# Performance work log

Measured on AMD Instinct MI355X. Metric: run time of the kernel, lower is better.

Reference implementation:

```python
import jax, jax.numpy as jnp
import numpy as np

L, B, E, H, NE, K = 1024, 8, 512, 8, 8, 2
HD = E // H
SLOPE = 0.01  # LeakyReLU default negative slope
EPS = 1e-5    # LayerNorm eps


def _lin(x, w, b):
    return x @ w.T + b


def _ln(x, g, b):
    m = x.mean(-1, keepdims=True)
    v = ((x - m) ** 2).mean(-1, keepdims=True)
    return (x - m) / jnp.sqrt(v + EPS) * g + b


def _leaky(x):
    return jnp.where(x >= 0, x, SLOPE * x)


def setup_inputs() -> dict:
    key = jax.random.key(0)
    ks = jax.random.split(key, 16)
    def n(k, shape, s=0.02):
        return (jax.random.normal(k, shape) * s).astype(jnp.float32)
    z = lambda *s: jnp.zeros(s, jnp.float32)
    o = lambda *s: jnp.ones(s, jnp.float32)
    return {
        "x": jax.random.normal(ks[0], (L, B, E), jnp.float32),
        "wq": n(ks[1], (E, E)), "bq": z(E),
        "wk": n(ks[2], (E, E)), "bk": z(E),
        "wv": n(ks[3], (E, E)), "bv": z(E),
        "in_w": n(ks[4], (3 * E, E)), "in_b": z(3 * E),
        "out_w": n(ks[5], (E, E)), "out_b": z(E),
        "ln1_g": o(E), "ln1_b": z(E),
        "ln2_g": o(E), "ln2_b": z(E),
        "sh_w": n(ks[6], (E, E)), "sh_b": z(E),
        "gate_w": n(ks[7], (NE, E)), "gate_b": z(NE),
        "exp_w": n(ks[8], (NE, E, E)), "exp_b": z(NE, E),
    }


def reference(x, wq, bq, wk, bk, wv, bv, in_w, in_b, out_w, out_b,
              ln1_g, ln1_b, ln2_g, ln2_b, sh_w, sh_b,
              gate_w, gate_b, exp_w, exp_b):
    # --- outer QKV projections (to_q/to_k/to_v) ---
    q = _lin(x, wq, bq); k = _lin(x, wk, bk); v = _lin(x, wv, bv)
    # --- nn.MultiheadAttention internal in_proj + SDPA + out_proj ---
    wqi, wki, wvi = jnp.split(in_w, 3, axis=0)
    bqi, bki, bvi = jnp.split(in_b, 3)
    q = _lin(q, wqi, bqi); k = _lin(k, wki, bki); v = _lin(v, wvi, bvi)
    heads = lambda t: t.reshape(L, B, H, HD).transpose(1, 2, 0, 3)  # (B,H,L,HD)
    qh, kh, vh = heads(q), heads(k), heads(v)
    att = jax.nn.softmax(
        jnp.einsum('bhqd,bhkd->bhqk', qh, kh) / np.float32(np.sqrt(HD)), axis=-1)
    ao = jnp.einsum('bhqk,bhkd->bhqd', att, vh).transpose(2, 0, 1, 3).reshape(L, B, E)
    ao = _lin(ao, out_w, out_b)
    x1 = _ln(x + ao, ln1_g, ln1_b)
    # --- top-k MoE (vectorized dense expert eval + gather/combine) ---
    probs = jax.nn.softmax(_lin(x1, gate_w, gate_b), axis=-1)     # (L,B,NE)
    topv, topi = jax.lax.top_k(probs, K)                          # (L,B,K)
    wts = topv / topv.sum(-1, keepdims=True)
    allout = _leaky(jnp.einsum('lbe,noe->lbno', x1, exp_w) + exp_b)  # (L,B,NE,E)
    sel = jnp.take_along_axis(allout, jnp.broadcast_to(topi[..., None], (L, B, K, E)), axis=2)
    moe_out = (wts[..., None] * sel).sum(axis=2)                  # (L,B,E)
    # Switch-style load-balance auxiliary loss
    mask = jax.nn.one_hot(topi, NE, dtype=x1.dtype).sum(axis=2)   # (L,B,NE)
    f = mask.reshape(-1, NE).mean(0)
    P = probs.reshape(-1, NE).mean(0)
    gating_loss = NE * jnp.sum(f * P)
    # --- shared expert + residual + LN ---
    shared = _leaky(_lin(x1, sh_w, sh_b))
    x2 = _ln(x1 + moe_out + shared, ln2_g, ln2_b)
    return (x2, gating_loss)
```

## Files before the change

### kernel.cpp

```cpp
#include <hip/hip_runtime.h>
#include <stdint.h>

#define LL   1024
#define BB   8
#define EE   512
#define HH   8
#define HDD  64
#define NEXP 8
#define TT   8192

typedef unsigned short u16t;
typedef __bf16 bf16x8 __attribute__((ext_vector_type(8)));
typedef u16t   u16x8  __attribute__((ext_vector_type(8)));
typedef u16t   u16x4  __attribute__((ext_vector_type(4)));
typedef float  f32x4  __attribute__((ext_vector_type(4)));

#define LAM 0.18033688011112042f

__device__ __forceinline__ u16t f2bf(float f) {
  union { float f; unsigned int u; } a; a.f = f;
  unsigned int r = a.u + 0x7fffu + ((a.u >> 16) & 1u);
  return (u16t)(r >> 16);
}
__device__ __forceinline__ float bf2f(u16t s) {
  union { unsigned int u; float f; } a; a.u = ((unsigned int)s) << 16; return a.f;
}

__device__ __forceinline__ f32x4 mfma16(bf16x8 a, bf16x8 b, f32x4 c) {
  return __builtin_amdgcn_mfma_f32_16x16x32_bf16(a, b, c, 0, 0, 0);
}

#define GLDS16(gp, lp) \
  __builtin_amdgcn_global_load_lds( \
      (const __attribute__((address_space(1))) unsigned int*)(const void*)(gp), \
      (__attribute__((address_space(3))) unsigned int*)(void*)(lp), 16, 0, 0)

__global__ __launch_bounds__(256) void cvt_all(
    const float* __restrict__ x, const float* __restrict__ in_w,
    const float* __restrict__ out_w, const float* __restrict__ shw,
    const float* __restrict__ expw,
    u16t* __restrict__ xb, u16t* __restrict__ inwb, u16t* __restrict__ outwb,
    u16t* __restrict__ shwb, u16t* __restrict__ expwb) {
  const int bid = blockIdx.x;
  const float* s; u16t* d; int i;
  if (bid < 4096)      { s = x;     d = xb;    i = bid; }
  else if (bid < 4864) { s = in_w;  d = inwb;  i = bid - 4096; }
  else if (bid < 5120) { s = out_w; d = outwb; i = bid - 4864; }
  else if (bid < 5376) { s = shw;   d = shwb;  i = bid - 5120; }
  else                 { s = expw;  d = expwb; i = bid - 5376; }
  const int idx = (i * 256 + threadIdx.x) * 4;
  float4 v = *(const float4*)&s[idx];
  u16x4 o = { f2bf(v.x), f2bf(v.y), f2bf(v.z), f2bf(v.w) };
  *(u16x4*)&d[idx] = o;
}

__global__ __launch_bounds__(256) void cvt_t(const float* __restrict__ w0,
                                             const float* __restrict__ w1,
                                             const float* __restrict__ w2,
                                             u16t* __restrict__ out) {
  const float* src = blockIdx.z == 0 ? w0 : blockIdx.z == 1 ? w1 : w2;
  u16t* dst = out + (size_t)blockIdx.z * 262144;
  __shared__ float tile[64][65];
  const int r = threadIdx.x >> 4;
  const int c = (threadIdx.x & 15) * 4;
  const int r0 = blockIdx.y * 64, c0 = blockIdx.x * 64;
#pragma unroll
  for (int i = 0; i < 4; i++) {
    float4 v = *(const float4*)&src[(size_t)(r0 + r + i * 16) * 512 + c0 + c];
    tile[r + i * 16][c] = v.x; tile[r + i * 16][c + 1] = v.y;
    tile[r + i * 16][c + 2] = v.z; tile[r + i * 16][c + 3] = v.w;
  }
  __syncthreads();
#pragma unroll
  for (int i = 0; i < 4; i++) {
    const int orow = c0 + r + i * 16;
    u16x4 o = { f2bf(tile[c][r + i * 16]), f2bf(tile[c + 1][r + i * 16]),
                f2bf(tile[c + 2][r + i * 16]), f2bf(tile[c + 3][r + i * 16]) };
    *(u16x4*)&dst[(size_t)orow * 512 + r0 + c] = o;
  }
}

__global__ __launch_bounds__(256) void compose_k(const u16t* __restrict__ Aall,
                                                 const u16t* __restrict__ Wall,
                                                 u16t* __restrict__ Call) {
  const u16t* A = Aall + (size_t)blockIdx.z * 262144;
  const u16t* W = Wall + (size_t)blockIdx.z * 262144;
  u16t* C = Call + (size_t)blockIdx.z * 262144;
  const float scale = blockIdx.z == 0 ? LAM : 1.0f;
  __shared__ alignas(16) u16t As[64 * 32];
  __shared__ alignas(16) u16t Ws[64 * 32];
  const int tid = threadIdx.x;
  const int lane = tid & 63, wave = tid >> 6;
  const int r15 = lane & 15, rhi = lane >> 4;
  const int wr = wave >> 1, wc = wave & 1;
  const int m0 = blockIdx.x * 64, n0 = blockIdx.y * 64;
  const int arow = tid >> 2, acol = (tid & 3) * 8;
  const f32x4 fz = {0.f, 0.f, 0.f, 0.f};
  f32x4 acc[2][2] = {{fz, fz}, {fz, fz}};
  const u16t* Ap = A + (size_t)(m0 + arow) * 512 + acol;
  const u16t* Wp = W + (size_t)(n0 + arow) * 512 + acol;
  u16t* As0 = &As[tid * 8];
  u16t* Ws0 = &Ws[tid * 8];
  for (int kt = 0; kt < 512; kt += 32) {
    __syncthreads();
    GLDS16(Ap + kt, As0);
    GLDS16(Wp + kt, Ws0);
    asm volatile("s_waitcnt vmcnt(0)" ::: "memory");
    __syncthreads();
    bf16x8 af[2], bfv[2];
#pragma unroll
    for (int mi = 0; mi < 2; mi++)
      af[mi] = *(const bf16x8*)&As[(wr * 32 + mi * 16 + r15) * 32 + rhi * 8];
#pragma unroll
    for (int ni = 0; ni < 2; ni++)
      bfv[ni] = *(const bf16x8*)&Ws[(wc * 32 + ni * 16 + r15) * 32 + rhi * 8];
#pragma unroll
    for (int mi = 0; mi < 2; mi++)
#pragma unroll
      for (int ni = 0; ni < 2; ni++)
        acc[mi][ni] = mfma16(af[mi], bfv[ni], acc[mi][ni]);
  }
#pragma unroll
  for (int mi = 0; mi < 2; mi++)
#pragma unroll
    for (int ni = 0; ni < 2; ni++) {
      const int col = n0 + wc * 32 + ni * 16 + r15;
#pragma unroll
      for (int r = 0; r < 4; r++) {
        const int row = m0 + wr * 32 + mi * 16 + rhi * 4 + r;
        C[(size_t)row * 512 + col] = f2bf(acc[mi][ni][r] * scale);
      }
    }
}

__global__ __launch_bounds__(256) void bias_mv(const float* __restrict__ in_w,
                                               const float* __restrict__ in_b,
                                               const float* __restrict__ b0,
                                               const float* __restrict__ b1,
                                               const float* __restrict__ b2v,
                                               float* __restrict__ out) {
  const int bi = blockIdx.x;
  const int seg = bi >> 3, m0 = (bi & 7) * 64;
  const float* bvec = seg == 0 ? b0 : seg == 1 ? b1 : b2v;
  const int m = m0 + (threadIdx.x >> 2), q = threadIdx.x & 3;
  const float* row = in_w + (size_t)(seg * 512 + m) * 512 + q * 128;
  const float* bv = bvec + q * 128;
  float s = 0.f;
  for (int j = 0; j < 128; j++) s += row[j] * bv[j];
  s += __shfl_xor(s, 1); s += __shfl_xor(s, 2);
  if (q == 0) {
    float r2 = s + in_b[seg * 512 + m];
    out[seg * 512 + m] = seg == 0 ? r2 * LAM : r2;
  }
}

template<int ACT, int OUTBF>
__global__ __launch_bounds__(256) void gemm_bt(
    const u16t* __restrict__ A, int lda,
    const u16t* __restrict__ W,
    const float* __restrict__ bias,
    void* __restrict__ Cp, int ldc, int K)
{
  __shared__ alignas(16) u16t As[128 * 32];
  __shared__ alignas(16) u16t Ws[128 * 32];
  const int tid  = threadIdx.x;
  const int lane = tid & 63, wave = tid >> 6;
  const int r15  = lane & 15, rhi = lane >> 4;
  const int wr   = wave >> 1, wc  = wave & 1;
  const int m0 = blockIdx.x * 128, n0 = blockIdx.y * 128;
  const int arow = tid >> 2, acol = (tid & 3) * 8;

  const f32x4 fz = {0.f, 0.f, 0.f, 0.f};
  f32x4 acc[4][4];
#pragma unroll
  for (int i = 0; i < 4; i++)
#pragma unroll
    for (int j = 0; j < 4; j++) acc[i][j] = fz;

  const u16t* Ap0 = A + (size_t)(m0 + arow) * lda + acol;
  const u16t* Ap1 = A + (size_t)(m0 + arow + 64) * lda + acol;
  const u16t* Wp0 = W + (size_t)(n0 + arow) * K + acol;
  const u16t* Wp1 = W + (size_t)(n0 + arow + 64) * K + acol;
  u16t* As0 = &As[tid * 8];       u16t* As1 = &As[(tid + 256) * 8];
  u16t* Ws0 = &Ws[tid * 8];       u16t* Ws1 = &Ws[(tid + 256) * 8];

  for (int kt = 0; kt < K; kt += 32) {
    __syncthreads();
    GLDS16(Ap0 + kt, As0);
    GLDS16(Ap1 + kt, As1);
    GLDS16(Wp0 + kt, Ws0);
    GLDS16(Wp1 + kt, Ws1);
    asm volatile("s_waitcnt vmcnt(0)" ::: "memory");
    __syncthreads();
    bf16x8 af[4], bfv[4];
#pragma unroll
    for (int mi = 0; mi < 4; mi++)
      af[mi] = *(const bf16x8*)&As[(wr * 64 + mi * 16 + r15) * 32 + rhi * 8];
#pragma unroll
    for (int ni = 0; ni < 4; ni++)
      bfv[ni] = *(const bf16x8*)&Ws[(wc * 64 + ni * 16 + r15) * 32 + rhi * 8];
#pragma unroll
    for (int mi = 0; mi < 4; mi++)
#pragma unroll
      for (int ni = 0; ni < 4; ni++)
        acc[mi][ni] = mfma16(af[mi], bfv[ni], acc[mi][ni]);
  }

#pragma unroll
  for (int mi = 0; mi < 4; mi++) {
#pragma unroll
    for (int ni = 0; ni < 4; ni++) {
      const int col = n0 + wc * 64 + ni * 16 + r15;
      const float bv = bias[col];
#pragma unroll
      for (int r = 0; r < 4; r++) {
        const int row = m0 + wr * 64 + mi * 16 + rhi * 4 + r;
        float v = acc[mi][ni][r] + bv;
        if (ACT == 1) v = v >= 0.f ? v : 0.01f * v;
        if (OUTBF) ((u16t*)Cp)[(size_t)row * ldc + col] = f2bf(v);
        else       ((float*)Cp)[(size_t)row * ldc + col] = v;
      }
    }
  }
}

template<int ACT>
__global__ __launch_bounds__(256) void gemm64(
    const u16t* __restrict__ A, int lda,
    const u16t* __restrict__ W,
    const float* __restrict__ bias,
    u16t* __restrict__ Cp, int ldc, int K)
{
  __shared__ alignas(16) u16t As[64 * 32];
  __shared__ alignas(16) u16t Ws[64 * 32];
  const int tid  = threadIdx.x;
  const int lane = tid & 63, wave = tid >> 6;
  const int r15  = lane & 15, rhi = lane >> 4;
  const int wr   = wave >> 1, wc  = wave & 1;
  const int m0 = blockIdx.x * 64, n0 = blockIdx.y * 64;
  const int arow = tid >> 2, acol = (tid & 3) * 8;

  const f32x4 fz = {0.f, 0.f, 0.f, 0.f};
  f32x4 acc[2][2] = {{fz, fz}, {fz, fz}};

  const u16t* Ap = A + (size_t)(m0 + arow) * lda + acol;
  const u16t* Wp = W + (size_t)(n0 + arow) * K + acol;
  u16t* As0 = &As[tid * 8];
  u16t* Ws0 = &Ws[tid * 8];

  for (int kt = 0; kt < K; kt += 32) {
    __syncthreads();
    GLDS16(Ap + kt, As0);
    GLDS16(Wp + kt, Ws0);
    asm volatile("s_waitcnt vmcnt(0)" ::: "memory");
    __syncthreads();
    bf16x8 af[2], bfv[2];
#pragma unroll
    for (int mi = 0; mi < 2; mi++)
      af[mi] = *(const bf16x8*)&As[(wr * 32 + mi * 16 + r15) * 32 + rhi * 8];
#pragma unroll
    for (int ni = 0; ni < 2; ni++)
      bfv[ni] = *(const bf16x8*)&Ws[(wc * 32 + ni * 16 + r15) * 32 + rhi * 8];
#pragma unroll
    for (int mi = 0; mi < 2; mi++)
#pragma unroll
      for (int ni = 0; ni < 2; ni++)
        acc[mi][ni] = mfma16(af[mi], bfv[ni], acc[mi][ni]);
  }

#pragma unroll
  for (int mi = 0; mi < 2; mi++)
#pragma unroll
    for (int ni = 0; ni < 2; ni++) {
      const int col = n0 + wc * 32 + ni * 16 + r15;
      const float bv = bias[col];
#pragma unroll
      for (int r = 0; r < 4; r++) {
        const int row = m0 + wr * 32 + mi * 16 + rhi * 4 + r;
        float v = acc[mi][ni][r] + bv;
        if (ACT == 1) v = v >= 0.f ? v : 0.01f * v;
        Cp[(size_t)row * ldc + col] = f2bf(v);
      }
    }
}

#define MOE_MAX_TILES 200
__global__ __launch_bounds__(256) void moe_shared(
    const u16t* __restrict__ x1b, const u16t* __restrict__ expwb,
    const float* __restrict__ expb,
    const u16t* __restrict__ shwb, const float* __restrict__ shb,
    const int* __restrict__ counts,
    const int* __restrict__ list, const float* __restrict__ wlist,
    u16t* __restrict__ out_slots, u16t* __restrict__ shrd)
{
  const int idx = blockIdx.x;
  int e = 0, base = 0, cnt = 0;
  for (; e < 8; e++) {
    cnt = counts[e];
    const int nt = (cnt + 127) >> 7;
    if (idx < base + nt) break;
    base += nt;
  }
  const bool sh = (e == 8);
  if (sh) {
    cnt = TT;
    if (idx - base >= 64) return;
  }
  const int m0 = (idx - base) * 128;
  if (m0 >= cnt) return;

  const int n0 = blockIdx.y * 128;
  __shared__ alignas(16) u16t As[128 * 32];
  __shared__ alignas(16) u16t Ws[128 * 32];
  __shared__ int tks[128];
  __shared__ float wws[128];
  const int tid  = threadIdx.x;
  const int lane = tid & 63, wave = tid >> 6;
  const int r15  = lane & 15, rhi = lane >> 4;
  const int wr   = wave >> 1, wc  = wave & 1;
  const int arow = tid >> 2, acol = (tid & 3) * 8;

  if (tid < 128) {
    if (sh) { tks[tid] = m0 + tid; wws[tid] = 1.f; }
    else {
      int i2 = m0 + tid; if (i2 >= cnt) i2 = cnt - 1;
      tks[tid] = list[e * 8192 + i2];
      wws[tid] = wlist[e * 8192 + i2];
    }
  }
  __syncthreads();
  const int tokA = sh ? tks[arow] : (tks[arow] >> 1);
  const int tokB = sh ? tks[arow + 64] : (tks[arow + 64] >> 1);

  const f32x4 fz = {0.f, 0.f, 0.f, 0.f};
  f32x4 acc[4][4];
#pragma unroll
  for (int i = 0; i < 4; i++)
#pragma unroll
    for (int j = 0; j < 4; j++) acc[i][j] = fz;

  const u16t* Ap0 = x1b + (size_t)tokA * 512 + acol;
  const u16t* Ap1 = x1b + (size_t)tokB * 512 + acol;
  const u16t* W  = (sh ? shwb : expwb + (size_t)e * 262144);
  const float* bias = sh ? shb : expb + e * 512;
  u16t* outp = sh ? shrd : out_slots;
  const u16t* Wp0 = W + (size_t)(n0 + arow) * 512 + acol;
  const u16t* Wp1 = Wp0 + (size_t)64 * 512;
  u16t* As0 = &As[tid * 8];  u16t* As1 = &As[(tid + 256) * 8];
  u16t* Ws0 = &Ws[tid * 8];  u16t* Ws1 = &Ws[(tid + 256) * 8];

  for (int kt = 0; kt < 512; kt += 32) {
    __syncthreads();
    GLDS16(Ap0 + kt, As0);
    GLDS16(Ap1 + kt, As1);
    GLDS16(Wp0 + kt, Ws0);
    GLDS16(Wp1 + kt, Ws1);
    asm volatile("s_waitcnt vmcnt(0)" ::: "memory");
    __syncthreads();
    bf16x8 af[4], bfv[4];
#pragma unroll
    for (int mi = 0; mi < 4; mi++)
      af[mi] = *(const bf16x8*)&As[(wr * 64 + mi * 16 + r15) * 32 + rhi * 8];
#pragma unroll
    for (int ni = 0; ni < 4; ni++)
      bfv[ni] = *(const bf16x8*)&Ws[(wc * 64 + ni * 16 + r15) * 32 + rhi * 8];
#pragma unroll
    for (int mi = 0; mi < 4; mi++)
#pragma unroll
      for (int ni = 0; ni < 4; ni++)
        acc[mi][ni] = mfma16(af[mi], bfv[ni], acc[mi][ni]);
  }

#pragma unroll
  for (int mi = 0; mi < 4; mi++)
#pragma unroll
    for (int ni = 0; ni < 4; ni++) {
      const int col = n0 + wc * 64 + ni * 16 + r15;
      const float bv = bias[col];
#pragma unroll
      for (int r = 0; r < 4; r++) {
        const int rl = wr * 64 + mi * 16 + rhi * 4 + r;
        if (m0 + rl < cnt) {
          float z = acc[mi][ni][r] + bv;
          z = z >= 0.f ? z : 0.01f * z;
          outp[(size_t)tks[rl] * 512 + col] = f2bf(wws[rl] * z);
        }
      }
    }
}

__global__ __launch_bounds__(512) void attn_kernel(
    const u16t* __restrict__ qkv, u16t* __restrict__ ao)
{
  const int bh = blockIdx.x;
  const int b = bh >> 3, h = bh & 7;
  const int qg = blockIdx.y;
  const int tid  = threadIdx.x;
  const int lane = tid & 63, wave = tid >> 6;
  const int r15  = lane & 15, rhi = lane >> 4;

  __shared__ alignas(16) u16t Ks[128 * 72];
  __shared__ alignas(16) u16t Vt[64 * 136];

  const int qrow = qg * 128 + (wave >> 2) * 64 + (wave & 3) * 16 + r15;
  const size_t qoff = ((size_t)qrow * BB + b) * 1536 + h * HDD;
  const bf16x8 qf0 = *(const bf16x8*)&qkv[qoff + rhi * 8];
  const bf16x8 qf1 = *(const bf16x8*)&qkv[qoff + 32 + rhi * 8];

  const f32x4 fz = {0.f, 0.f, 0.f, 0.f};
  f32x4 oa[4] = {fz, fz, fz, fz};
  float psum = 0.f;

  const int krow = tid >> 2, kchunk = (tid & 3) * 16;
  const int vd0 = (wave & 3) * 16 + (lane >> 5) * 8;
  const int vkv = (wave >> 2) * 64 + (lane & 31) * 2;

  u16x8 kA0, kA1, vA0, vA1;
  {
    const size_t kb = ((size_t)krow * BB + b) * 1536 + h * HDD + 512 + kchunk;
    kA0 = *(const u16x8*)&qkv[kb];
    kA1 = *(const u16x8*)&qkv[kb + 8];
    const size_t v0 = ((size_t)vkv * BB + b) * 1536 + h * HDD + 1024 + vd0;
    vA0 = *(const u16x8*)&qkv[v0];
    vA1 = *(const u16x8*)&qkv[v0 + (size_t)BB * 1536];
  }

  for (int t = 0; t < 8; t++) {
    __syncthreads();
    {
      u16t* kd = &Ks[krow * 72 + kchunk];
      *(u16x8*)&kd[0] = kA0;
      *(u16x8*)&kd[8] = kA1;
    }
#pragma unroll
    for (int j = 0; j < 8; j++) {
      unsigned int w = (unsigned int)vA0[j] | ((unsigned int)vA1[j] << 16);
      *(unsigned int*)&Vt[(vd0 + j) * 136 + vkv] = w;
    }
    if (t < 7) {
      const int kv0n = (t + 1) * 128;
      const size_t kb = ((size_t)(kv0n + krow) * BB + b) * 1536 + h * HDD + 512 + kchunk;
      kA0 = *(const u16x8*)&qkv[kb];
      kA1 = *(const u16x8*)&qkv[kb + 8];
      const size_t v0 = ((size_t)(kv0n + vkv) * BB + b) * 1536 + h * HDD + 1024 + vd0;
      vA0 = *(const u16x8*)&qkv[v0];
      vA1 = *(const u16x8*)&qkv[v0 + (size_t)BB * 1536];
    }
    __syncthreads();

    f32x4 s[8];
    __builtin_amdgcn_s_setprio(1);
#pragma unroll
    for (int nt = 0; nt < 8; nt++) {
      const u16t* kr = &Ks[(nt * 16 + r15) * 72];
      bf16x8 k0 = *(const bf16x8*)&kr[rhi * 8];
      bf16x8 k1 = *(const bf16x8*)&kr[32 + rhi * 8];
      f32x4 acc = fz;
      acc = mfma16(k0, qf0, acc);
      acc = mfma16(k1, qf1, acc);
      s[nt] = acc;
    }
    __builtin_amdgcn_s_setprio(0);

    unsigned int P2[8][2];
#pragma unroll
    for (int nt = 0; nt < 8; nt++) {
#pragma unroll
      for (int r = 0; r < 4; r++) {
        s[nt][r] = exp2f(s[nt][r]);
        psum += s[nt][r];
      }
      asm("v_cvt_pk_bf16_f32 %0, %1, %2" : "=v"(P2[nt][0]) : "v"(s[nt][0]), "v"(s[nt][1]));
      asm("v_cvt_pk_bf16_f32 %0, %1, %2" : "=v"(P2[nt][1]) : "v"(s[nt][2]), "v"(s[nt][3]));
    }

    __builtin_amdgcn_s_setprio(1);
#pragma unroll
    for (int c = 0; c < 4; c++) {
      union { unsigned int w[4]; bf16x8 v; } pf;
      pf.w[0] = P2[2 * c][0];     pf.w[1] = P2[2 * c][1];
      pf.w[2] = P2[2 * c + 1][0]; pf.w[3] = P2[2 * c + 1][1];
#pragma unroll
      for (int dd = 0; dd < 4; dd++) {
        const u16t* vr = &Vt[(dd * 16 + r15) * 136 + c * 32 + rhi * 4];
        union { u16x4 h[2]; bf16x8 v; } vb;
        vb.h[0] = *(const u16x4*)&vr[0];
        vb.h[1] = *(const u16x4*)&vr[16];
        oa[dd] = mfma16(vb.v, pf.v, oa[dd]);
      }
    }
    __builtin_amdgcn_s_setprio(0);
  }

  float ls = psum;
  ls += __shfl_xor(ls, 16);
  ls += __shfl_xor(ls, 32);
  const float inv = 1.f / ls;
  const size_t obase = ((size_t)qrow * BB + b) * EE + h * HDD;
#pragma unroll
  for (int dd = 0; dd < 4; dd++) {
    u16x4 o = { f2bf(oa[dd][0] * inv), f2bf(oa[dd][1] * inv),
                f2bf(oa[dd][2] * inv), f2bf(oa[dd][3] * inv) };
    *(u16x4*)&ao[obase + dd * 16 + rhi * 4] = o;
  }
}

__device__ __forceinline__ float wave_sum(float v) {
#pragma unroll
  for (int off = 1; off < 64; off <<= 1) v += __shfl_xor(v, off);
  return v;
}

__global__ __launch_bounds__(256) void ln1_gate(
    const float* __restrict__ x, const u16t* __restrict__ aopb,
    const float* __restrict__ g, const float* __restrict__ be,
    const float* __restrict__ gw, const float* __restrict__ gb,
    u16t* __restrict__ x1b,
    int* __restrict__ tok_pack, float2* __restrict__ tok_w,
    float* __restrict__ partials)
{
  const int wave = threadIdx.x >> 6, lane = threadIdx.x & 63;
  const int t = blockIdx.x * 4 + wave;
  const size_t base = (size_t)t * EE + lane * 8;
  float4 a0 = *(const float4*)&x[base], a1 = *(const float4*)&x[base + 4];
  u16x8 ap = *(const u16x8*)&aopb[base];
  float v[8] = { a0.x + bf2f(ap[0]), a0.y + bf2f(ap[1]), a0.z + bf2f(ap[2]), a0.w + bf2f(ap[3]),
                 a1.x + bf2f(ap[4]), a1.y + bf2f(ap[5]), a1.z + bf2f(ap[6]), a1.w + bf2f(ap[7]) };
  float s = 0.f;
#pragma unroll
  for (int i = 0; i < 8; i++) s += v[i];
  const float mean = wave_sum(s) * (1.f / EE);
  float vs = 0.f;
#pragma unroll
  for (int i = 0; i < 8; i++) { v[i] -= mean; vs += v[i] * v[i]; }
  const float inv = rsqrtf(wave_sum(vs) * (1.f / EE) + 1e-5f);
  float4 g0 = *(const float4*)&g[lane * 8],  g1 = *(const float4*)&g[lane * 8 + 4];
  float4 b0 = *(const float4*)&be[lane * 8], b1 = *(const float4*)&be[lane * 8 + 4];
  float o[8] = { v[0]*inv*g0.x + b0.x, v[1]*inv*g0.y + b0.y, v[2]*inv*g0.z + b0.z, v[3]*inv*g0.w + b0.w,
                 v[4]*inv*g1.x + b1.x, v[5]*inv*g1.y + b1.y, v[6]*inv*g1.z + b1.z, v[7]*inv*g1.w + b1.w };
  u16x8 ob = { f2bf(o[0]), f2bf(o[1]), f2bf(o[2]), f2bf(o[3]),
               f2bf(o[4]), f2bf(o[5]), f2bf(o[6]), f2bf(o[7]) };
  *(u16x8*)&x1b[base] = ob;

  float pe[8];
  float mx = -1e30f;
#pragma unroll
  for (int e = 0; e < 8; e++) {
    float4 ga = *(const float4*)&gw[e * EE + lane * 8];
    float4 gB = *(const float4*)&gw[e * EE + lane * 8 + 4];
    float d = o[0]*ga.x + o[1]*ga.y + o[2]*ga.z + o[3]*ga.w
            + o[4]*gB.x + o[5]*gB.y + o[6]*gB.z + o[7]*gB.w;
#pragma unroll
    for (int off = 1; off < 64; off <<= 1) d += __shfl_xor(d, off);
    pe[e] = d + gb[e];
    mx = fmaxf(mx, pe[e]);
  }
  float se = 0.f;
#pragma unroll
  for (int e = 0; e < 8; e++) { pe[e] = __expf(pe[e] - mx); se += pe[e]; }
  const float invs = 1.f / se;
#pragma unroll
  for (int e = 0; e < 8; e++) pe[e] *= invs;
  float v1 = -1.f; int i1 = 0;
#pragma unroll
  for (int e = 0; e < 8; e++) if (pe[e] > v1) { v1 = pe[e]; i1 = e; }
  float v2 = -1.f; int i2 = -1;
#pragma unroll
  for (int e = 0; e < 8; e++) if (e != i1 && pe[e] > v2) { v2 = pe[e]; i2 = e; }
  const float denom = 1.f / (v1 + v2);
  if (lane == 0) {
    tok_pack[t] = i1 | (i2 << 8);
    float2 w; w.x = v1 * denom; w.y = v2 * denom;
    tok_w[t] = w;
  }
  __shared__ float fb[4][8], pb[4][8];
  if (lane < 8) {
    fb[wave][lane] = (lane == i1 || lane == i2) ? 1.f : 0.f;
    pb[wave][lane] = pe[lane];
  }
  __syncthreads();
  if (threadIdx.x < 8) {
    const int e = threadIdx.x;
    partials[(size_t)blockIdx.x * 16 + e]     = fb[0][e] + fb[1][e] + fb[2][e] + fb[3][e];
    partials[(size_t)blockIdx.x * 16 + 8 + e] = pb[0][e] + pb[1][e] + pb[2][e] + pb[3][e];
  }
}

__global__ __launch_bounds__(256) void ln2_kernel(
    const u16t* __restrict__ x1b, const u16t* __restrict__ slots,
    const u16t* __restrict__ sh,
    const float* __restrict__ g, const float* __restrict__ be,
    float* __restrict__ out)
{
  const int wave = threadIdx.x >> 6, lane = threadIdx.x & 63;
  const int t = blockIdx.x * 4 + wave;
  const size_t base = (size_t)t * EE + lane * 8;
  u16x8 xv = *(const u16x8*)&x1b[base];
  u16x8 m0 = *(const u16x8*)&slots[(size_t)(2 * t) * EE + lane * 8];
  u16x8 m1 = *(const u16x8*)&slots[(size_t)(2 * t + 1) * EE + lane * 8];
  u16x8 sv = *(const u16x8*)&sh[base];
  float v[8];
#pragma unroll
  for (int i = 0; i < 8; i++)
    v[i] = bf2f(xv[i]) + bf2f(m0[i]) + bf2f(m1[i]) + bf2f(sv[i]);
  float s = 0.f;
#pragma unroll
  for (int i = 0; i < 8; i++) s += v[i];
  const float mean = wave_sum(s) * (1.f / EE);
  float vs = 0.f;
#pragma unroll
  for (int i = 0; i < 8; i++) { v[i] -= mean; vs += v[i] * v[i]; }
  const float inv = rsqrtf(wave_sum(vs) * (1.f / EE) + 1e-5f);
  float4 g0 = *(const float4*)&g[lane * 8],  g1 = *(const float4*)&g[lane * 8 + 4];
  float4 b0 = *(const float4*)&be[lane * 8], b1 = *(const float4*)&be[lane * 8 + 4];
  *(float4*)&out[base] = make_float4(v[0]*inv*g0.x + b0.x, v[1]*inv*g0.y + b0.y,
                                     v[2]*inv*g0.z + b0.z, v[3]*inv*g0.w + b0.w);
  *(float4*)&out[base + 4] = make_float4(v[4]*inv*g1.x + b1.x, v[5]*inv*g1.y + b1.y,
                                         v[6]*inv*g1.z + b1.z, v[7]*inv*g1.w + b1.w);
}

__global__ __launch_bounds__(512) void build_lists(
    const int* __restrict__ tok_pack, const float2* __restrict__ tok_w,
    int* __restrict__ counts, int* __restrict__ list, float* __restrict__ wlist,
    const float* __restrict__ partials, float* __restrict__ loss_out)
{
  if (blockIdx.x == 8) {
    __shared__ float acc2[32][16];
    __shared__ float fin[16];
    const int c = threadIdx.x & 15, grp = threadIdx.x >> 4;
    float s = 0.f;
    for (int i = grp; i < 2048; i += 32) s += partials[(size_t)i * 16 + c];
    acc2[grp][c] = s;
    __syncthreads();
    if (threadIdx.x < 16) {
      float t2 = 0.f;
      for (int g2 = 0; g2 < 32; g2++) t2 += acc2[g2][threadIdx.x];
      fin[threadIdx.x] = t2;
    }
    __syncthreads();
    if (threadIdx.x == 0) {
      float loss = 0.f;
      for (int e = 0; e < 8; e++)
        loss += (fin[e] * (1.f / TT)) * (fin[8 + e] * (1.f / TT));
      loss_out[0] = loss * 8.f;
    }
    return;
  }
  const int e = blockIdx.x;
  const int tid = threadIdx.x;
  const int lane = tid & 63, wave = tid >> 6;
  __shared__ int wtot[8];
  __shared__ int runb;
  if (tid == 0) runb = 0;
  __syncthreads();
  for (int c = 0; c < 16; c++) {
    const int t = c * 512 + tid;
    const int pk = tok_pack[t];
    const int i1 = pk & 255, i2 = (pk >> 8) & 255;
    const bool s1 = (i1 == e);
    const bool flag = s1 || (i2 == e);
    const unsigned long long mask = __ballot(flag);
    if (lane == 63) wtot[wave] = __popcll(mask);
    __syncthreads();
    int wbase = 0;
#pragma unroll
    for (int w2 = 0; w2 < 8; w2++) if (w2 < wave) wbase += wtot[w2];
    int btot = 0;
#pragma unroll
    for (int w2 = 0; w2 < 8; w2++) btot += wtot[w2];
    if (flag) {
      const int pre = __popcll(mask & ((1ull << lane) - 1ull));
      const int pos = runb + wbase + pre;
      list[e * 8192 + pos] = 2 * t + (s1 ? 0 : 1);
      float2 w = tok_w[t];
      wlist[e * 8192 + pos] = s1 ? w.x : w.y;
    }
    __syncthreads();
    if (tid == 0) runb += btot;
    __syncthreads();
  }
  if (tid == 0) counts[e] = runb;
}

extern "C" void kernel_launch(void* const* d_in, const int* in_sizes, int n_in,
                              void* d_out, int out_size, void* d_ws, size_t ws_size,
                              hipStream_t stream) {
  const float* x    = (const float*)d_in[0];
  const float* wq   = (const float*)d_in[1];
  const float* bq   = (const float*)d_in[2];
  const float* wk   = (const float*)d_in[3];
  const float* bk   = (const float*)d_in[4];
  const float* wv   = (const float*)d_in[5];
  const float* bv   = (const float*)d_in[6];
  const float* in_w = (const float*)d_in[7];
  const float* in_b = (const float*)d_in[8];
  const float* out_w= (const float*)d_in[9];
  const float* out_b= (const float*)d_in[10];
  const float* ln1g = (const float*)d_in[11];
  const float* ln1b = (const float*)d_in[12];
  const float* ln2g = (const float*)d_in[13];
  const float* ln2b = (const float*)d_in[14];
  const float* shw  = (const float*)d_in[15];
  const float* shb  = (const float*)d_in[16];
  const float* gw   = (const float*)d_in[17];
  const float* gb   = (const float*)d_in[18];
  const float* expw = (const float*)d_in[19];
  const float* expb = (const float*)d_in[20];

  char* ws = (char*)d_ws;
  u16t* xb     = (u16t*)(ws + 0);
  u16t* inwb   = (u16t*)(ws + 8388608);
  u16t* w3t    = (u16t*)(ws + 9961472);
  u16t* w2big  = (u16t*)(ws + 11534336);
  u16t* outwb  = (u16t*)(ws + 13107200);
  u16t* shwb   = (u16t*)(ws + 13631488);
  u16t* expwb  = (u16t*)(ws + 14155776);
  float* b2    = (float*)(ws + 18350080);
  int*  tok_pack = (int*)(ws + 18356224);
  float2* tok_w  = (float2*)(ws + 18388992);
  int*  counts = (int*)(ws + 18454528);
  int*  list   = (int*)(ws + 18454656);
  float* wlist = (float*)(ws + 18716800);
  float* parts = (float*)(ws + 18978944);
  const size_t S = 19110016;
  u16t* qkvb   = (u16t*)(ws + S);
  u16t* aopb   = (u16t*)(ws + S);
  u16t* x1b    = (u16t*)(ws + S + 16777216);
  u16t* oslots = (u16t*)(ws + S);
  u16t* aob    = (u16t*)(ws + 0);
  u16t* shrd   = (u16t*)(ws + 0);
  float* outp  = (float*)d_out;

  dim3 blk(256);
  cvt_all<<<7424, blk, 0, stream>>>(x, in_w, out_w, shw, expw,
                                    xb, inwb, outwb, shwb, expwb);
  cvt_t<<<dim3(8, 8, 3), blk, 0, stream>>>(wq, wk, wv, w3t);
  compose_k<<<dim3(8, 8, 3), blk, 0, stream>>>(inwb, w3t, w2big);
  bias_mv<<<24, blk, 0, stream>>>(in_w, in_b, bq, bk, bv, b2);
  gemm_bt<0,1><<<dim3(64, 12), blk, 0, stream>>>(xb, EE, w2big, b2, qkvb, 1536, EE);
  attn_kernel<<<dim3(64, 8), dim3(512), 0, stream>>>(qkvb, aob);
  gemm64<0><<<dim3(128, 8), blk, 0, stream>>>(aob, EE, outwb, out_b, aopb, EE, EE);
  ln1_gate<<<2048, blk, 0, stream>>>(x, aopb, ln1g, ln1b, gw, gb, x1b, tok_pack, tok_w, parts);
  build_lists<<<9, dim3(512), 0, stream>>>(tok_pack, tok_w, counts, list, wlist,
                                           parts, outp + (size_t)TT * EE);
  moe_shared<<<dim3(MOE_MAX_TILES, 4), blk, 0, stream>>>(x1b, expwb, expb, shwb, shb,
                                                         counts, list, wlist, oslots, shrd);
  ln2_kernel<<<2048, blk, 0, stream>>>(x1b, oslots, shrd, ln2g, ln2b, outp);
}
```

Baseline: 174.4 us.

## Double-buffer LDS tiles in GEMM kernels and fold transpose-convert into cvt_all

The three GEMM kernels (gemm_bt, gemm64, moe_shared) now use two LDS buffers and issue the next k-tile's global-to-LDS loads before computing on the current one, waiting with a partial vmcnt. This overlaps memory latency with MFMA work, which was previously serialized by a full wait every iteration. Separately, the wq/wk/wv transpose-convert kernel is merged into cvt_all as extra blocks, removing one launch. Doubling the shared memory may lower occupancy, and the merged kernel now allocates a 64x65 float tile in every block.

After: 170.8 us (median of 3 runs). 1.02x faster.

```diff
diff --git a/kernel.cpp b/kernel.cpp
--- a/kernel.cpp
+++ b/kernel.cpp
@@ -39,9 +39,37 @@
     const float* __restrict__ x, const float* __restrict__ in_w,
     const float* __restrict__ out_w, const float* __restrict__ shw,
     const float* __restrict__ expw,
+    const float* __restrict__ wq, const float* __restrict__ wk,
+    const float* __restrict__ wv,
     u16t* __restrict__ xb, u16t* __restrict__ inwb, u16t* __restrict__ outwb,
-    u16t* __restrict__ shwb, u16t* __restrict__ expwb) {
+    u16t* __restrict__ shwb, u16t* __restrict__ expwb, u16t* __restrict__ w3t) {
+  __shared__ float tile[64][65];
   const int bid = blockIdx.x;
+  if (bid >= 7424) {
+    const int i = bid - 7424;
+    const int z = i >> 6, rem = i & 63;
+    const int by = rem >> 3, bx = rem & 7;
+    const float* src = z == 0 ? wq : z == 1 ? wk : wv;
+    u16t* dst = w3t + (size_t)z * 262144;
+    const int r = threadIdx.x >> 4;
+    const int c = (threadIdx.x & 15) * 4;
+    const int r0 = by * 64, c0 = bx * 64;
+#pragma unroll
+    for (int k = 0; k < 4; k++) {
+      float4 v = *(const float4*)&src[(size_t)(r0 + r + k * 16) * 512 + c0 + c];
+      tile[r + k * 16][c] = v.x; tile[r + k * 16][c + 1] = v.y;
+      tile[r + k * 16][c + 2] = v.z; tile[r + k * 16][c + 3] = v.w;
+    }
+    __syncthreads();
+#pragma unroll
+    for (int k = 0; k < 4; k++) {
+      const int orow = c0 + r + k * 16;
+      u16x4 o = { f2bf(tile[c][r + k * 16]), f2bf(tile[c + 1][r + k * 16]),
+                  f2bf(tile[c + 2][r + k * 16]), f2bf(tile[c + 3][r + k * 16]) };
+      *(u16x4*)&dst[(size_t)orow * 512 + r0 + c] = o;
+    }
+    return;
+  }
   const float* s; u16t* d; int i;
   if (bid < 4096)      { s = x;     d = xb;    i = bid; }
   else if (bid < 4864) { s = in_w;  d = inwb;  i = bid - 4096; }
@@ -52,32 +80,6 @@
   float4 v = *(const float4*)&s[idx];
   u16x4 o = { f2bf(v.x), f2bf(v.y), f2bf(v.z), f2bf(v.w) };
   *(u16x4*)&d[idx] = o;
-}
-
-__global__ __launch_bounds__(256) void cvt_t(const float* __restrict__ w0,
-                                             const float* __restrict__ w1,
-                                             const float* __restrict__ w2,
-                                             u16t* __restrict__ out) {
-  const float* src = blockIdx.z == 0 ? w0 : blockIdx.z == 1 ? w1 : w2;
-  u16t* dst = out + (size_t)blockIdx.z * 262144;
-  __shared__ float tile[64][65];
-  const int r = threadIdx.x >> 4;
-  const int c = (threadIdx.x & 15) * 4;
-  const int r0 = blockIdx.y * 64, c0 = blockIdx.x * 64;
-#pragma unroll
-  for (int i = 0; i < 4; i++) {
-    float4 v = *(const float4*)&src[(size_t)(r0 + r + i * 16) * 512 + c0 + c];
-    tile[r + i * 16][c] = v.x; tile[r + i * 16][c + 1] = v.y;
-    tile[r + i * 16][c + 2] = v.z; tile[r + i * 16][c + 3] = v.w;
-  }
-  __syncthreads();
-#pragma unroll
-  for (int i = 0; i < 4; i++) {
-    const int orow = c0 + r + i * 16;
-    u16x4 o = { f2bf(tile[c][r + i * 16]), f2bf(tile[c + 1][r + i * 16]),
-                f2bf(tile[c + 2][r + i * 16]), f2bf(tile[c + 3][r + i * 16]) };
-    *(u16x4*)&dst[(size_t)orow * 512 + r0 + c] = o;
-  }
 }
 
 __global__ __launch_bounds__(256) void compose_k(const u16t* __restrict__ Aall,
@@ -161,8 +163,8 @@
     const float* __restrict__ bias,
     void* __restrict__ Cp, int ldc, int K)
 {
-  __shared__ alignas(16) u16t As[128 * 32];
-  __shared__ alignas(16) u16t Ws[128 * 32];
+  __shared__ alignas(16) u16t As[2 * 128 * 32];
+  __shared__ alignas(16) u16t Ws[2 * 128 * 32];
   const int tid  = threadIdx.x;
   const int lane = tid & 63, wave = tid >> 6;
   const int r15  = lane & 15, rhi = lane >> 4;
@@ -181,29 +183,41 @@
   const u16t* Ap1 = A + (size_t)(m0 + arow + 64) * lda + acol;
   const u16t* Wp0 = W + (size_t)(n0 + arow) * K + acol;
   const u16t* Wp1 = W + (size_t)(n0 + arow + 64) * K + acol;
-  u16t* As0 = &As[tid * 8];       u16t* As1 = &As[(tid + 256) * 8];
-  u16t* Ws0 = &Ws[tid * 8];       u16t* Ws1 = &Ws[(tid + 256) * 8];
-
+
+  GLDS16(Ap0, &As[tid * 8]);
+  GLDS16(Ap1, &As[(tid + 256) * 8]);
+  GLDS16(Wp0, &Ws[tid * 8]);
+  GLDS16(Wp1, &Ws[(tid + 256) * 8]);
+
+  int cur = 0;
   for (int kt = 0; kt < K; kt += 32) {
-    __syncthreads();
-    GLDS16(Ap0 + kt, As0);
-    GLDS16(Ap1 + kt, As1);
-    GLDS16(Wp0 + kt, Ws0);
-    GLDS16(Wp1 + kt, Ws1);
-    asm volatile("s_waitcnt vmcnt(0)" ::: "memory");
-    __syncthreads();
+    const int nxt = cur ^ 1;
+    if (kt) __syncthreads();
+    if (kt + 32 < K) {
+      const int no = nxt * 4096;
+      GLDS16(Ap0 + kt + 32, &As[no + tid * 8]);
+      GLDS16(Ap1 + kt + 32, &As[no + (tid + 256) * 8]);
+      GLDS16(Wp0 + kt + 32, &Ws[no + tid * 8]);
+      GLDS16(Wp1 + kt + 32, &Ws[no + (tid + 256) * 8]);
+      asm volatile("s_waitcnt vmcnt(4)" ::: "memory");
+    } else {
+      asm volatile("s_waitcnt vmcnt(0)" ::: "memory");
+    }
+    __syncthreads();
+    const int cb = cur * 4096;
     bf16x8 af[4], bfv[4];
 #pragma unroll
     for (int mi = 0; mi < 4; mi++)
-      af[mi] = *(const bf16x8*)&As[(wr * 64 + mi * 16 + r15) * 32 + rhi * 8];
+      af[mi] = *(const bf16x8*)&As[cb + (wr * 64 + mi * 16 + r15) * 32 + rhi * 8];
 #pragma unroll
     for (int ni = 0; ni < 4; ni++)
-      bfv[ni] = *(const bf16x8*)&Ws[(wc * 64 + ni * 16 + r15) * 32 + rhi * 8];
+      bfv[ni] = *(const bf16x8*)&Ws[cb + (wc * 64 + ni * 16 + r15) * 32 + rhi * 8];
 #pragma unroll
     for (int mi = 0; mi < 4; mi++)
 #pragma unroll
       for (int ni = 0; ni < 4; ni++)
         acc[mi][ni] = mfma16(af[mi], bfv[ni], acc[mi][ni]);
+    cur = nxt;
   }
 
 #pragma unroll
@@ -231,8 +245,8 @@
     const float* __restrict__ bias,
     u16t* __restrict__ Cp, int ldc, int K)
 {
-  __shared__ alignas(16) u16t As[64 * 32];
-  __shared__ alignas(16) u16t Ws[64 * 32];
+  __shared__ alignas(16) u16t As[2 * 64 * 32];
+  __shared__ alignas(16) u16t Ws[2 * 64 * 32];
   const int tid  = threadIdx.x;
   const int lane = tid & 63, wave = tid >> 6;
   const int r15  = lane & 15, rhi = lane >> 4;
@@ -245,27 +259,37 @@
 
   const u16t* Ap = A + (size_t)(m0 + arow) * lda + acol;
   const u16t* Wp = W + (size_t)(n0 + arow) * K + acol;
-  u16t* As0 = &As[tid * 8];
-  u16t* Ws0 = &Ws[tid * 8];
-
+
+  GLDS16(Ap, &As[tid * 8]);
+  GLDS16(Wp, &Ws[tid * 8]);
+
+  int cur = 0;
   for (int kt = 0; kt < K; kt += 32) {
-    __syncthreads();
-    GLDS16(Ap + kt, As0);
-    GLDS16(Wp + kt, Ws0);
-    asm volatile("s_waitcnt vmcnt(0)" ::: "memory");
-    __syncthreads();
+    const int nxt = cur ^ 1;
+    if (kt) __syncthreads();
+    if (kt + 32 < K) {
+      const int no = nxt * 2048;
+      GLDS16(Ap + kt + 32, &As[no + tid * 8]);
+      GLDS16(Wp + kt + 32, &Ws[no + tid * 8]);
+      asm volatile("s_waitcnt vmcnt(2)" ::: "memory");
+    } else {
+      asm volatile("s_waitcnt vmcnt(0)" ::: "memory");
+    }
+    __syncthreads();
+    const int cb = cur * 2048;
     bf16x8 af[2], bfv[2];
 #pragma unroll
     for (int mi = 0; mi < 2; mi++)
-      af[mi] = *(const bf16x8*)&As[(wr * 32 + mi * 16 + r15) * 32 + rhi * 8];
+      af[mi] = *(const bf16x8*)&As[cb + (wr * 32 + mi * 16 + r15) * 32 + rhi * 8];
 #pragma unroll
     for (int ni = 0; ni < 2; ni++)
-      bfv[ni] = *(const bf16x8*)&Ws[(wc * 32 + ni * 16 + r15) * 32 + rhi * 8];
+      bfv[ni] = *(const bf16x8*)&Ws[cb + (wc * 32 + ni * 16 + r15) * 32 + rhi * 8];
 #pragma unroll
     for (int mi = 0; mi < 2; mi++)
 #pragma unroll
       for (int ni = 0; ni < 2; ni++)
         acc[mi][ni] = mfma16(af[mi], bfv[ni], acc[mi][ni]);
+    cur = nxt;
   }
 
 #pragma unroll
@@ -310,8 +334,8 @@
   if (m0 >= cnt) return;
 
   const int n0 = blockIdx.y * 128;
-  __shared__ alignas(16) u16t As[128 * 32];
-  __shared__ alignas(16) u16t Ws[128 * 32];
+  __shared__ alignas(16) u16t As[2 * 128 * 32];
+  __shared__ alignas(16) u16t Ws[2 * 128 * 32];
   __shared__ int tks[128];
   __shared__ float wws[128];
   const int tid  = threadIdx.x;
@@ -346,29 +370,41 @@
   u16t* outp = sh ? shrd : out_slots;
   const u16t* Wp0 = W + (size_t)(n0 + arow) * 512 + acol;
   const u16t* Wp1 = Wp0 + (size_t)64 * 512;
-  u16t* As0 = &As[tid * 8];  u16t* As1 = &As[(tid + 256) * 8];
-  u16t* Ws0 = &Ws[tid * 8];  u16t* Ws1 = &Ws[(tid + 256) * 8];
-
+
+  GLDS16(Ap0, &As[tid * 8]);
+  GLDS16(Ap1, &As[(tid + 256) * 8]);
+  GLDS16(Wp0, &Ws[tid * 8]);
+  GLDS16(Wp1, &Ws[(tid + 256) * 8]);
+
+  int cur = 0;
   for (int kt = 0; kt < 512; kt += 32) {
-    __syncthreads();
-    GLDS16(Ap0 + kt, As0);
-    GLDS16(Ap1 + kt, As1);
-    GLDS16(Wp0 + kt, Ws0);
-    GLDS16(Wp1 + kt, Ws1);
-    asm volatile("s_waitcnt vmcnt(0)" ::: "memory");
-    __syncthreads();
+    const int nxt = cur ^ 1;
+    if (kt) __syncthreads();
+    if (kt + 32 < 512) {
+      const int no = nxt * 4096;
+      GLDS16(Ap0 + kt + 32, &As[no + tid * 8]);
+      GLDS16(Ap1 + kt + 32, &As[no + (tid + 256) * 8]);
+      GLDS16(Wp0 + kt + 32, &Ws[no + tid * 8]);
+      GLDS16(Wp1 + kt + 32, &Ws[no + (tid + 256) * 8]);
+      asm volatile("s_waitcnt vmcnt(4)" ::: "memory");
+    } else {
+      asm volatile("s_waitcnt vmcnt(0)" ::: "memory");
+    }
+    __syncthreads();
+    const int cb = cur * 4096;
     bf16x8 af[4], bfv[4];
 #pragma unroll
     for (int mi = 0; mi < 4; mi++)
-      af[mi] = *(const bf16x8*)&As[(wr * 64 + mi * 16 + r15) * 32 + rhi * 8];
+      af[mi] = *(const bf16x8*)&As[cb + (wr * 64 + mi * 16 + r15) * 32 + rhi * 8];
 #pragma unroll
     for (int ni = 0; ni < 4; ni++)
-      bfv[ni] = *(const bf16x8*)&Ws[(wc * 64 + ni * 16 + r15) * 32 + rhi * 8];
+      bfv[ni] = *(const bf16x8*)&Ws[cb + (wc * 64 + ni * 16 + r15) * 32 + rhi * 8];
 #pragma unroll
     for (int mi = 0; mi < 4; mi++)
 #pragma unroll
       for (int ni = 0; ni < 4; ni++)
         acc[mi][ni] = mfma16(af[mi], bfv[ni], acc[mi][ni]);
+    cur = nxt;
   }
 
 #pragma unroll
@@ -732,9 +768,8 @@
   float* outp  = (float*)d_out;
 
   dim3 blk(256);
-  cvt_all<<<7424, blk, 0, stream>>>(x, in_w, out_w, shw, expw,
-                                    xb, inwb, outwb, shwb, expwb);
-  cvt_t<<<dim3(8, 8, 3), blk, 0, stream>>>(wq, wk, wv, w3t);
+  cvt_all<<<7616, blk, 0, stream>>>(x, in_w, out_w, shw, expw, wq, wk, wv,
+                                    xb, inwb, outwb, shwb, expwb, w3t);
   compose_k<<<dim3(8, 8, 3), blk, 0, stream>>>(inwb, w3t, w2big);
   bias_mv<<<24, blk, 0, stream>>>(in_w, in_b, bq, bk, bv, b2);
   gemm_bt<0,1><<<dim3(64, 12), blk, 0, stream>>>(xb, EE, w2big, b2, qkvb, 1536, EE);
```
